# Performance work log

Measured on AMD Instinct MI355X. Metric: run time of the kernel, lower is better.

The kernel has to match this reference:

```python
import jax, jax.numpy as jnp
import numpy as np

E = 8        # num_experts (material buckets)
L1 = 3072    # input dim
L2 = 15
L3 = 32
RF = 32      # ROUTER_FEATURES_PER_PERSPECTIVE
B = 16384
AUX_ALPHA = 0.01
Z_ALPHA = 0.001
LOAD_FLOOR = 0.05
LOAD_CAP = 0.5
PROBE_ALPHA = 0.01
PROBE_TAU = 1.0
PROBE_THRESH = 0.05
TEACHER_ALPHA = 0.0   # initial value of _teacher_alpha buffer
SCORE_SCALE = 600.0
SQ_SCALE = 255.0 / 256.0


def setup_inputs() -> dict:
    key = jax.random.key(0)
    ks = jax.random.split(key, 12)
    x = jax.random.uniform(ks[0], (B, L1), dtype=jnp.float32)
    ls_indices = jax.random.randint(ks[1], (B,), 0, E)
    psqt = jax.random.normal(ks[2], (B,), dtype=jnp.float32)
    score_target = jax.random.normal(ks[3], (B,), dtype=jnp.float32)
    router_w = 0.1 * jax.random.normal(ks[4], (E, 2 * RF), dtype=jnp.float32)
    router_b = jnp.zeros((E,), dtype=jnp.float32)
    # effective (coalesced) expert params, per _expert_params view
    w1 = jax.random.normal(ks[5], (E, L2 + 1, L1), dtype=jnp.float32) / np.sqrt(L1)
    b1 = 0.01 * jax.random.normal(ks[6], (E, L2 + 1), dtype=jnp.float32)
    w2 = jax.random.normal(ks[7], (E, L3, 2 * L2), dtype=jnp.float32) / np.sqrt(2 * L2)
    b2 = 0.01 * jax.random.normal(ks[8], (E, L3), dtype=jnp.float32)
    w3 = jax.random.normal(ks[9], (E, 1, L3), dtype=jnp.float32) / np.sqrt(L3)
    b3 = jnp.zeros((E, 1), dtype=jnp.float32)  # output bias zeroed in __init__
    return {"x": x, "ls_indices": ls_indices, "psqt": psqt,
            "score_target": score_target, "router_w": router_w,
            "router_b": router_b, "w1": w1, "b1": b1, "w2": w2, "b2": b2,
            "w3": w3, "b3": b3}


def _forward(x, psqt, score_target, router_w, router_b, w1, b1, w2, b2, w3, b3, ls_indices):
    half = L1 // 2
    router_in = jnp.concatenate([x[:, :RF], x[:, half:half + RF]], axis=1)  # [B, 64]
    gate_logits = router_in @ router_w.T + router_b                          # [B, E]
    logp = jax.nn.log_softmax(gate_logits, axis=-1)
    gate_probs = jnp.exp(logp)
    expert_indices = jnp.argmax(gate_logits, axis=-1)                        # [B]

    teacher_ce = -jnp.mean(jnp.take_along_axis(logp, ls_indices[:, None], axis=1))
    frac = jnp.bincount(expert_indices, length=E).astype(gate_probs.dtype) / gate_probs.shape[0]
    avg_gate = gate_probs.mean(axis=0)
    load = avg_gate + jax.lax.stop_gradient(frac - avg_gate)
    floor_loss = jnp.mean(jnp.square(jnp.maximum(LOAD_FLOOR - load, 0.0)))
    cap_loss = jnp.mean(jnp.square(jnp.maximum(load - LOAD_CAP, 0.0)))
    aux_loss = floor_loss + cap_loss
    z_loss = jnp.mean(jnp.square(jax.nn.logsumexp(gate_logits, axis=-1)))

    # ---- all-experts stacked MLP (fusion target) ----
    l1c = jnp.einsum('bi,eoi->beo', x, w1) + b1          # [B, E, L2+1]
    a, a_skip = l1c[..., :L2], l1c[..., L2:]              # [B,E,L2], [B,E,1]
    h = jnp.clip(jnp.concatenate([a * a * SQ_SCALE, a], axis=-1), 0.0, 1.0)  # [B,E,2*L2]
    l2x = jnp.clip(jnp.einsum('bei,eoi->beo', h, w2) + b2, 0.0, 1.0)         # [B,E,L3]
    all_out = jnp.einsum('bei,eoi->beo', l2x, w3) + b3 + a_skip              # [B,E,1]

    # ---- probe loss ----
    probe_weight = PROBE_ALPHA * max(PROBE_THRESH - TEACHER_ALPHA, 0.0) / max(PROBE_THRESH, 1e-9)
    expert_out = (all_out[..., 0] + psqt[:, None]) * SCORE_SCALE             # [B, E]
    err = jnp.square(expert_out - score_target[:, None])
    err = err - err.min(axis=1, keepdims=True)
    pt = jax.nn.softmax(-jax.lax.stop_gradient(err) / PROBE_TAU, axis=-1)
    log_pt = jnp.log(jnp.maximum(pt, 1e-30))
    probe_loss = jnp.mean(jnp.sum(pt * (log_pt - logp), axis=-1))            # kl_div batchmean

    router_loss = (AUX_ALPHA * aux_loss + Z_ALPHA * z_loss
                   + TEACHER_ALPHA * teacher_ce + probe_weight * probe_loss)

    l3x = jnp.take_along_axis(all_out, expert_indices[:, None, None], axis=1)[:, 0, :]  # [B, 1]
    gp = jnp.take_along_axis(gate_probs, expert_indices[:, None], axis=1)               # [B, 1]
    l3x = l3x * (1.0 + gp - jax.lax.stop_gradient(gp))  # straight-through (training mode)
    return l3x, router_loss


def reference(x, ls_indices, psqt, score_target, router_w, router_b, w1, b1, w2, b2, w3, b3):
    return _forward(x, psqt, score_target, router_w, router_b, w1, b1, w2, b2, w3, b3, ls_indices)
```

## Files before the change

kernel.cpp:

```cpp
#include <hip/hip_runtime.h>
#include <math.h>

#define BATCH 16384
#define K_DIM 3072

typedef float  f32x4  __attribute__((ext_vector_type(4)));
typedef __bf16 bf16x8 __attribute__((ext_vector_type(8)));
typedef unsigned int u32x2 __attribute__((ext_vector_type(2)));

__device__ __forceinline__ unsigned short f2bf(float f) {
  union { float f; unsigned u; } v; v.f = f;
  unsigned u = v.u + 0x7fffu + ((v.u >> 16) & 1u);
  return (unsigned short)(u >> 16);
}

__device__ __forceinline__ bf16x8 cvt8(f32x4 lo, f32x4 hi) {
  bf16x8 r;
  r[0] = (__bf16)lo[0]; r[1] = (__bf16)lo[1]; r[2] = (__bf16)lo[2]; r[3] = (__bf16)lo[3];
  r[4] = (__bf16)hi[0]; r[5] = (__bf16)hi[1]; r[6] = (__bf16)hi[2]; r[7] = (__bf16)hi[3];
  return r;
}

__device__ __forceinline__ void gld16(const void* g, void* l) {
  __builtin_amdgcn_global_load_lds(
      (const __attribute__((address_space(1))) unsigned int*)g,
      (__attribute__((address_space(3))) unsigned int*)l, 16, 0, 0);
}

__global__ void cvt_w1_kernel(const float* __restrict__ w1, unsigned short* __restrict__ o,
                              float* __restrict__ accs) {
  if (blockIdx.x == 0 && threadIdx.x < 16) accs[threadIdx.x] = 0.f;
  int i = blockIdx.x * 256 + threadIdx.x;
  f32x4 v = ((const f32x4*)w1)[i];
  u32x2 p = { (unsigned)f2bf(v.x) | ((unsigned)f2bf(v.y) << 16),
              (unsigned)f2bf(v.z) | ((unsigned)f2bf(v.w) << 16) };
  ((u32x2*)o)[i] = p;
}

__global__ __launch_bounds__(256, 2) void moe_main_kernel(
    const float* __restrict__ x, const unsigned short* __restrict__ w1bf,
    const float* __restrict__ b1, const float* __restrict__ w2,
    const float* __restrict__ b2, const float* __restrict__ w3,
    const float* __restrict__ b3, const float* __restrict__ psqt,
    const float* __restrict__ st, const float* __restrict__ rw,
    const float* __restrict__ rb, float* __restrict__ out,
    float* __restrict__ accs) {
  __shared__ __align__(16) unsigned char stage_sm[73728];
  __shared__ int   hist[8];
  __shared__ float zred[4], wred[4];

  const int tid = threadIdx.x;
  const int bm  = blockIdx.x;
  float* Cl  = (float*)stage_sm;
  float* w2s = (float*)(stage_sm + 17024);

  if (tid < 8) hist[tid] = 0;
  __syncthreads();

  const int lane = tid & 63, wv = tid >> 6;
  const int l16 = lane & 15, lq = lane >> 4;
  const int rt = wv & 1;
  const int cb = (wv >> 1) << 2;

  const float* gA[2]; int lA[2];
#pragma unroll
  for (int r = 0; r < 2; ++r) {
    int idx = r * 256 + tid; int row = idx >> 4; int blk = idx & 15;
    gA[r] = x + (size_t)(bm * 32 + row) * K_DIM + ((blk ^ (row & 7)) << 2);
    lA[r] = idx << 4;
  }
  const unsigned short* gB[4]; int lB[4];
#pragma unroll
  for (int r = 0; r < 4; ++r) {
    int idx = r * 256 + tid; int row = idx >> 3; int blk = idx & 7;
    gB[r] = w1bf + (size_t)row * K_DIM + ((blk ^ (row & 7)) << 3);
    lB[r] = idx << 4;
  }

  const int arow = rt * 16 + l16;
  int aoff[2], boff[2][4];
#pragma unroll
  for (int ks = 0; ks < 2; ++ks) {
    aoff[ks] = arow * 256 + (((ks * 8 + lq * 2) ^ (arow & 7)) << 4);
#pragma unroll
    for (int cc = 0; cc < 4; ++cc) {
      int o = (cb + cc) * 16 + l16;
      boff[ks][cc] = o * 128 + (((lq + ks * 4) ^ (l16 & 7)) << 4);
    }
  }

#define STAGE(C, KT) do {                                                  \
    unsigned char* ab_ = stage_sm + (C) * 24576;                           \
    unsigned char* bb_ = ab_ + 8192;                                       \
    gld16(gA[0] + (KT) * 64, ab_ + lA[0]);                                 \
    gld16(gA[1] + (KT) * 64, ab_ + lA[1]);                                 \
    gld16(gB[0] + (KT) * 64, bb_ + lB[0]);                                 \
    gld16(gB[1] + (KT) * 64, bb_ + lB[1]);                                 \
    gld16(gB[2] + (KT) * 64, bb_ + lB[2]);                                 \
    gld16(gB[3] + (KT) * 64, bb_ + lB[3]);                                 \
  } while (0)

#define COMPUTE(C) do {                                                    \
    const unsigned char* ab_ = stage_sm + (C) * 24576;                     \
    const unsigned char* bb_ = ab_ + 8192;                                 \
    _Pragma("unroll")                                                      \
    for (int ks = 0; ks < 2; ++ks) {                                       \
      f32x4 a0 = *(const f32x4*)(ab_ + aoff[ks]);                          \
      f32x4 a1 = *(const f32x4*)(ab_ + (aoff[ks] ^ 16));                   \
      bf16x8 af = cvt8(a0, a1);                                            \
      _Pragma("unroll")                                                    \
      for (int cc = 0; cc < 4; ++cc) {                                     \
        bf16x8 bfv = *(const bf16x8*)(bb_ + boff[ks][cc]);                 \
        acc[cc] = __builtin_amdgcn_mfma_f32_16x16x32_bf16(af, bfv,         \
                                                          acc[cc], 0,0,0); \
      }                                                                    \
    }                                                                      \
  } while (0)

#define PH(C, T) do {                                                      \
    STAGE(((C) + 2) % 3, (T) + 2);                                         \
    asm volatile("s_waitcnt vmcnt(12)" ::: "memory");                      \
    __builtin_amdgcn_s_barrier();                                          \
    COMPUTE(C);                                                            \
    __builtin_amdgcn_s_barrier();                                          \
  } while (0)

  f32x4 acc[4];
#pragma unroll
  for (int cc = 0; cc < 4; ++cc) acc[cc] = (f32x4){0.f, 0.f, 0.f, 0.f};

  STAGE(0, 0);
  STAGE(1, 1);

  const int bl = tid >> 3, e = tid & 7;
  const int bg = bm * 32 + bl;
  const float* xrow  = x + (size_t)bg * K_DIM;
  const float* rwrow = rw + e * 64;
  double lr = (double)rb[e];
#pragma unroll
  for (int c4 = 0; c4 < 8; ++c4) {
    f32x4 xv = *(const f32x4*)(xrow + c4 * 4);
    f32x4 wvv = *(const f32x4*)(rwrow + c4 * 4);
#pragma unroll
    for (int j = 0; j < 4; ++j) lr = fma((double)xv[j], (double)wvv[j], lr);
  }
#pragma unroll
  for (int c4 = 0; c4 < 8; ++c4) {
    f32x4 xv = *(const f32x4*)(xrow + 1536 + c4 * 4);
    f32x4 wvv = *(const f32x4*)(rwrow + 32 + c4 * 4);
#pragma unroll
    for (int j = 0; j < 4; ++j) lr = fma((double)xv[j], (double)wvv[j], lr);
  }
  double mx = lr; int mi = e;
#pragma unroll
  for (int m = 1; m < 8; m <<= 1) {
    double ov = __shfl_xor(mx, m);
    int    oi = __shfl_xor(mi, m);
    if (ov > mx || (ov == mx && oi < mi)) { mx = ov; mi = oi; }
  }
  double ssum = exp(lr - mx);
#pragma unroll
  for (int m = 1; m < 8; m <<= 1) ssum += __shfl_xor(ssum, m);
  const double lse = mx + log(ssum);
  const float  logp_self = (float)(lr - lse);
  const int    rowEidx   = mi;

  if (e == 0) atomicAdd(&hist[rowEidx], 1);
  float zc = (e == 0) ? (float)(lse * lse) : 0.f;
#pragma unroll
  for (int m = 1; m < 64; m <<= 1) zc += __shfl_xor(zc, m);
  if (lane == 0) zred[wv] = zc;

#pragma unroll 1
  for (int kt = 0; kt < 45; kt += 3) {
    PH(0, kt);
    PH(1, kt + 1);
    PH(2, kt + 2);
  }
  PH(0, 45);
  asm volatile("s_waitcnt vmcnt(6)" ::: "memory");
  __builtin_amdgcn_s_barrier();
  COMPUTE(1);
  __builtin_amdgcn_s_barrier();
  asm volatile("s_waitcnt vmcnt(0)" ::: "memory");
  __builtin_amdgcn_s_barrier();
  COMPUTE(2);
  __builtin_amdgcn_s_barrier();

#pragma unroll
  for (int cc = 0; cc < 4; ++cc)
#pragma unroll
    for (int r = 0; r < 4; ++r)
      Cl[(rt * 16 + lq * 4 + r) * 132 + (cb + cc) * 16 + l16] = acc[cc][r];
  for (int i = tid; i < 7680; i += 256) {
    int ee = i / 960; int rr = i - ee * 960; int o = rr / 30; int ii = rr - o * 30;
    w2s[ee * 964 + ii * 32 + o] = w2[i];
  }
  __syncthreads();

  float a[16];
  {
    const float* crow = Cl + bl * 132 + e * 16;
    const float* b1p  = b1 + e * 16;
#pragma unroll
    for (int j = 0; j < 16; ++j) a[j] = crow[j] + b1p[j];
  }

  float h[30];
#pragma unroll
  for (int j = 0; j < 15; ++j) {
    float v = a[j];
    h[j]      = fminf(fmaxf(v * v * (255.0f / 256.0f), 0.f), 1.f);
    h[15 + j] = fminf(fmaxf(v, 0.f), 1.f);
  }

  float acc2[32];
  {
    const f32x4* b2v = (const f32x4*)(b2 + e * 32);
#pragma unroll
    for (int o4 = 0; o4 < 8; ++o4) {
      f32x4 t = b2v[o4];
      acc2[o4 * 4 + 0] = t.x; acc2[o4 * 4 + 1] = t.y;
      acc2[o4 * 4 + 2] = t.z; acc2[o4 * 4 + 3] = t.w;
    }
  }
  const f32x4* wrow = (const f32x4*)&w2s[e * 964];
#pragma unroll
  for (int i = 0; i < 30; ++i) {
    float hv = h[i];
#pragma unroll
    for (int o4 = 0; o4 < 8; ++o4) {
      f32x4 wq = wrow[i * 8 + o4];
      acc2[o4 * 4 + 0] += hv * wq.x;
      acc2[o4 * 4 + 1] += hv * wq.y;
      acc2[o4 * 4 + 2] += hv * wq.z;
      acc2[o4 * 4 + 3] += hv * wq.w;
    }
  }

  float outv = b3[e] + a[15];
  {
    const f32x4* w3v = (const f32x4*)(w3 + e * 32);
#pragma unroll
    for (int o4 = 0; o4 < 8; ++o4) {
      f32x4 t = w3v[o4];
      outv += fminf(fmaxf(acc2[o4 * 4 + 0], 0.f), 1.f) * t.x;
      outv += fminf(fmaxf(acc2[o4 * 4 + 1], 0.f), 1.f) * t.y;
      outv += fminf(fmaxf(acc2[o4 * 4 + 2], 0.f), 1.f) * t.z;
      outv += fminf(fmaxf(acc2[o4 * 4 + 3], 0.f), 1.f) * t.w;
    }
  }

  float eo  = (outv + psqt[bg]) * 600.0f;
  float dd  = eo - st[bg];
  float err = dd * dd;
  float mn = err;
  mn = fminf(mn, __shfl_xor(mn, 1));
  mn = fminf(mn, __shfl_xor(mn, 2));
  mn = fminf(mn, __shfl_xor(mn, 4));
  float wexp = expf(-(err - mn));
  float ss = wexp;
  ss += __shfl_xor(ss, 1); ss += __shfl_xor(ss, 2); ss += __shfl_xor(ss, 4);
  float pt  = wexp / ss;
  float lpt = logf(fmaxf(pt, 1e-30f));
  float term = pt * (lpt - logp_self);
  term += __shfl_xor(term, 1); term += __shfl_xor(term, 2); term += __shfl_xor(term, 4);
  float c1 = (e == 0) ? term : 0.f;
  c1 += __shfl_xor(c1, 8); c1 += __shfl_xor(c1, 16); c1 += __shfl_xor(c1, 32);
  if (lane == 0) wred[wv] = c1;

  if (e == rowEidx) out[bg] = outv;

  __syncthreads();
  if (tid == 0) {
    atomicAdd(&accs[8], zred[0] + zred[1] + zred[2] + zred[3]);
    atomicAdd(&accs[9], wred[0] + wred[1] + wred[2] + wred[3]);
  }
  if (tid < 8) atomicAdd(&accs[tid], (float)hist[tid]);
#undef STAGE
#undef COMPUTE
#undef PH
}

__global__ void finalize_kernel(const float* __restrict__ accs, float* __restrict__ out) {
  if (threadIdx.x == 0) {
    float fsum = 0.f;
    for (int e = 0; e < 8; ++e) {
      float frac = accs[e] * (1.0f / 16384.0f);
      float f = fmaxf(0.05f - frac, 0.f);
      float c = fmaxf(frac - 0.5f, 0.f);
      fsum += f * f + c * c;
    }
    float aux   = fsum * 0.125f;
    float z     = accs[8] * (1.0f / 16384.0f);
    float probe = accs[9] * (1.0f / 16384.0f);
    out[BATCH] = 0.01f * aux + 0.001f * z + 0.01f * probe;
  }
}

extern "C" void kernel_launch(void* const* d_in, const int* in_sizes, int n_in,
                              void* d_out, int out_size, void* d_ws, size_t ws_size,
                              hipStream_t stream) {
  const float* x    = (const float*)d_in[0];
  const float* psqt = (const float*)d_in[2];
  const float* st   = (const float*)d_in[3];
  const float* rw   = (const float*)d_in[4];
  const float* rb   = (const float*)d_in[5];
  const float* w1   = (const float*)d_in[6];
  const float* b1   = (const float*)d_in[7];
  const float* w2   = (const float*)d_in[8];
  const float* b2   = (const float*)d_in[9];
  const float* w3   = (const float*)d_in[10];
  const float* b3   = (const float*)d_in[11];
  float* out = (float*)d_out;

  unsigned short* w1bf = (unsigned short*)d_ws;
  float* accs = (float*)((char*)d_ws + 786432);

  cvt_w1_kernel<<<384, 256, 0, stream>>>(w1, w1bf, accs);
  moe_main_kernel<<<512, 256, 0, stream>>>(x, w1bf, b1, w2, b2, w3, b3,
                                           psqt, st, rw, rb, out, accs);
  finalize_kernel<<<1, 1, 0, stream>>>(accs, out);
}
```

Measured before the change: 332.3 us.

## Split block into producer and consumer warps for warp-specialized pipeline

Doubles the block to 512 threads: four producer waves issue the async global-to-LDS loads for the triple-buffered x/w1 tiles while four consumer waves run the MFMA compute and router. The point is to overlap memory issue with compute across separate waves instead of having every wave both load and compute. The cost is more threads per block, idle producer waves during the epilogue, and heavier register and occupancy pressure given the 72KB shared allocation. launch_bounds(512,4) cannot be met with that much LDS.

```diff
diff --git a/kernel.cpp b/kernel.cpp
--- a/kernel.cpp
+++ b/kernel.cpp
@@ -37,7 +37,7 @@
   ((u32x2*)o)[i] = p;
 }
 
-__global__ __launch_bounds__(256, 2) void moe_main_kernel(
+__global__ __launch_bounds__(512, 4) void moe_main_kernel(
     const float* __restrict__ x, const unsigned short* __restrict__ w1bf,
     const float* __restrict__ b1, const float* __restrict__ w2,
     const float* __restrict__ b2, const float* __restrict__ w3,
@@ -57,37 +57,15 @@
   if (tid < 8) hist[tid] = 0;
   __syncthreads();
 
-  const int lane = tid & 63, wv = tid >> 6;
-  const int l16 = lane & 15, lq = lane >> 4;
-  const int rt = wv & 1;
-  const int cb = (wv >> 1) << 2;
+  const int lane = tid & 63;
+  const bool isProd = (tid >= 256);
 
   const float* gA[2]; int lA[2];
-#pragma unroll
-  for (int r = 0; r < 2; ++r) {
-    int idx = r * 256 + tid; int row = idx >> 4; int blk = idx & 15;
-    gA[r] = x + (size_t)(bm * 32 + row) * K_DIM + ((blk ^ (row & 7)) << 2);
-    lA[r] = idx << 4;
-  }
   const unsigned short* gB[4]; int lB[4];
-#pragma unroll
-  for (int r = 0; r < 4; ++r) {
-    int idx = r * 256 + tid; int row = idx >> 3; int blk = idx & 7;
-    gB[r] = w1bf + (size_t)row * K_DIM + ((blk ^ (row & 7)) << 3);
-    lB[r] = idx << 4;
-  }
-
-  const int arow = rt * 16 + l16;
   int aoff[2], boff[2][4];
-#pragma unroll
-  for (int ks = 0; ks < 2; ++ks) {
-    aoff[ks] = arow * 256 + (((ks * 8 + lq * 2) ^ (arow & 7)) << 4);
-#pragma unroll
-    for (int cc = 0; cc < 4; ++cc) {
-      int o = (cb + cc) * 16 + l16;
-      boff[ks][cc] = o * 128 + (((lq + ks * 4) ^ (l16 & 7)) << 4);
-    }
-  }
+  f32x4 acc[4];
+  float logp_self = 0.f;
+  int   rowEidx   = 0;
 
 #define STAGE(C, KT) do {                                                  \
     unsigned char* ab_ = stage_sm + (C) * 24576;                           \
@@ -117,159 +95,196 @@
     }                                                                      \
   } while (0)
 
-#define PH(C, T) do {                                                      \
-    STAGE(((C) + 2) % 3, (T) + 2);                                         \
-    asm volatile("s_waitcnt vmcnt(12)" ::: "memory");                      \
-    __builtin_amdgcn_s_barrier();                                          \
-    COMPUTE(C);                                                            \
-    __builtin_amdgcn_s_barrier();                                          \
-  } while (0)
-
-  f32x4 acc[4];
-#pragma unroll
-  for (int cc = 0; cc < 4; ++cc) acc[cc] = (f32x4){0.f, 0.f, 0.f, 0.f};
-
-  STAGE(0, 0);
-  STAGE(1, 1);
-
-  const int bl = tid >> 3, e = tid & 7;
-  const int bg = bm * 32 + bl;
-  const float* xrow  = x + (size_t)bg * K_DIM;
-  const float* rwrow = rw + e * 64;
-  double lr = (double)rb[e];
-#pragma unroll
-  for (int c4 = 0; c4 < 8; ++c4) {
-    f32x4 xv = *(const f32x4*)(xrow + c4 * 4);
-    f32x4 wvv = *(const f32x4*)(rwrow + c4 * 4);
-#pragma unroll
-    for (int j = 0; j < 4; ++j) lr = fma((double)xv[j], (double)wvv[j], lr);
-  }
-#pragma unroll
-  for (int c4 = 0; c4 < 8; ++c4) {
-    f32x4 xv = *(const f32x4*)(xrow + 1536 + c4 * 4);
-    f32x4 wvv = *(const f32x4*)(rwrow + 32 + c4 * 4);
-#pragma unroll
-    for (int j = 0; j < 4; ++j) lr = fma((double)xv[j], (double)wvv[j], lr);
-  }
-  double mx = lr; int mi = e;
-#pragma unroll
-  for (int m = 1; m < 8; m <<= 1) {
-    double ov = __shfl_xor(mx, m);
-    int    oi = __shfl_xor(mi, m);
-    if (ov > mx || (ov == mx && oi < mi)) { mx = ov; mi = oi; }
-  }
-  double ssum = exp(lr - mx);
-#pragma unroll
-  for (int m = 1; m < 8; m <<= 1) ssum += __shfl_xor(ssum, m);
-  const double lse = mx + log(ssum);
-  const float  logp_self = (float)(lr - lse);
-  const int    rowEidx   = mi;
-
-  if (e == 0) atomicAdd(&hist[rowEidx], 1);
-  float zc = (e == 0) ? (float)(lse * lse) : 0.f;
-#pragma unroll
-  for (int m = 1; m < 64; m <<= 1) zc += __shfl_xor(zc, m);
-  if (lane == 0) zred[wv] = zc;
+  if (isProd) {
+    const int ptid = tid & 255;
+#pragma unroll
+    for (int r = 0; r < 2; ++r) {
+      int idx = r * 256 + ptid; int row = idx >> 4; int blk = idx & 15;
+      gA[r] = x + (size_t)(bm * 32 + row) * K_DIM + ((blk ^ (row & 7)) << 2);
+      lA[r] = idx << 4;
+    }
+#pragma unroll
+    for (int r = 0; r < 4; ++r) {
+      int idx = r * 256 + ptid; int row = idx >> 3; int blk = idx & 7;
+      gB[r] = w1bf + (size_t)row * K_DIM + ((blk ^ (row & 7)) << 3);
+      lB[r] = idx << 4;
+    }
+    STAGE(0, 0);
+    STAGE(1, 1);
+    asm volatile("s_waitcnt vmcnt(6)" ::: "memory");
+  } else {
+    const int cwv = tid >> 6;
+    const int l16 = lane & 15, lq = lane >> 4;
+    const int rt = cwv & 1;
+    const int cb = (cwv >> 1) << 2;
+    const int arow = rt * 16 + l16;
+#pragma unroll
+    for (int ks = 0; ks < 2; ++ks) {
+      aoff[ks] = arow * 256 + (((ks * 8 + lq * 2) ^ (arow & 7)) << 4);
+#pragma unroll
+      for (int cc = 0; cc < 4; ++cc) {
+        int o = (cb + cc) * 16 + l16;
+        boff[ks][cc] = o * 128 + (((lq + ks * 4) ^ (l16 & 7)) << 4);
+      }
+    }
+#pragma unroll
+    for (int cc = 0; cc < 4; ++cc) acc[cc] = (f32x4){0.f, 0.f, 0.f, 0.f};
+
+    const int bl = tid >> 3, e = tid & 7;
+    const int bg = bm * 32 + bl;
+    const float* xrow  = x + (size_t)bg * K_DIM;
+    const float* rwrow = rw + e * 64;
+    double lr = (double)rb[e];
+#pragma unroll
+    for (int c4 = 0; c4 < 8; ++c4) {
+      f32x4 xv  = *(const f32x4*)(xrow + c4 * 4);
+      f32x4 wvv = *(const f32x4*)(rwrow + c4 * 4);
+#pragma unroll
+      for (int j = 0; j < 4; ++j) lr = fma((double)xv[j], (double)wvv[j], lr);
+    }
+#pragma unroll
+    for (int c4 = 0; c4 < 8; ++c4) {
+      f32x4 xv  = *(const f32x4*)(xrow + 1536 + c4 * 4);
+      f32x4 wvv = *(const f32x4*)(rwrow + 32 + c4 * 4);
+#pragma unroll
+      for (int j = 0; j < 4; ++j) lr = fma((double)xv[j], (double)wvv[j], lr);
+    }
+    double mx = lr; int mi = e;
+#pragma unroll
+    for (int m = 1; m < 8; m <<= 1) {
+      double ov = __shfl_xor(mx, m);
+      int    oi = __shfl_xor(mi, m);
+      if (ov > mx || (ov == mx && oi < mi)) { mx = ov; mi = oi; }
+    }
+    double ssum = exp(lr - mx);
+#pragma unroll
+    for (int m = 1; m < 8; m <<= 1) ssum += __shfl_xor(ssum, m);
+    const double lse = mx + log(ssum);
+    logp_self = (float)(lr - lse);
+    rowEidx   = mi;
+
+    if (e == 0) atomicAdd(&hist[rowEidx], 1);
+    float zc = (e == 0) ? (float)(lse * lse) : 0.f;
+#pragma unroll
+    for (int m = 1; m < 64; m <<= 1) zc += __shfl_xor(zc, m);
+    if (lane == 0) zred[cwv] = zc;
+  }
 
 #pragma unroll 1
-  for (int kt = 0; kt < 45; kt += 3) {
-    PH(0, kt);
-    PH(1, kt + 1);
-    PH(2, kt + 2);
-  }
-  PH(0, 45);
-  asm volatile("s_waitcnt vmcnt(6)" ::: "memory");
+  for (int base = 0; base < 45; base += 3) {
+    __builtin_amdgcn_s_barrier();
+    if (isProd) { STAGE(2, base + 2); asm volatile("s_waitcnt vmcnt(6)" ::: "memory"); }
+    else        COMPUTE(0);
+    __builtin_amdgcn_s_barrier();
+    if (isProd) { STAGE(0, base + 3); asm volatile("s_waitcnt vmcnt(6)" ::: "memory"); }
+    else        COMPUTE(1);
+    __builtin_amdgcn_s_barrier();
+    if (isProd) { STAGE(1, base + 4); asm volatile("s_waitcnt vmcnt(6)" ::: "memory"); }
+    else        COMPUTE(2);
+  }
   __builtin_amdgcn_s_barrier();
-  COMPUTE(1);
+  if (isProd) { STAGE(2, 47); asm volatile("s_waitcnt vmcnt(6)" ::: "memory"); }
+  else        COMPUTE(0);
   __builtin_amdgcn_s_barrier();
-  asm volatile("s_waitcnt vmcnt(0)" ::: "memory");
+  if (isProd) { asm volatile("s_waitcnt vmcnt(0)" ::: "memory"); }
+  else        COMPUTE(1);
   __builtin_amdgcn_s_barrier();
-  COMPUTE(2);
-  __builtin_amdgcn_s_barrier();
-
-#pragma unroll
-  for (int cc = 0; cc < 4; ++cc)
-#pragma unroll
-    for (int r = 0; r < 4; ++r)
-      Cl[(rt * 16 + lq * 4 + r) * 132 + (cb + cc) * 16 + l16] = acc[cc][r];
-  for (int i = tid; i < 7680; i += 256) {
+  if (!isProd) COMPUTE(2);
+
+  __syncthreads();
+  if (!isProd) {
+    const int cwv = tid >> 6;
+    const int l16 = lane & 15, lq = lane >> 4;
+    const int rt = cwv & 1, cb = (cwv >> 1) << 2;
+#pragma unroll
+    for (int cc = 0; cc < 4; ++cc)
+#pragma unroll
+      for (int r = 0; r < 4; ++r)
+        Cl[(rt * 16 + lq * 4 + r) * 132 + (cb + cc) * 16 + l16] = acc[cc][r];
+  }
+  for (int i = tid; i < 7680; i += 512) {
     int ee = i / 960; int rr = i - ee * 960; int o = rr / 30; int ii = rr - o * 30;
     w2s[ee * 964 + ii * 32 + o] = w2[i];
   }
   __syncthreads();
 
-  float a[16];
-  {
-    const float* crow = Cl + bl * 132 + e * 16;
-    const float* b1p  = b1 + e * 16;
-#pragma unroll
-    for (int j = 0; j < 16; ++j) a[j] = crow[j] + b1p[j];
-  }
-
-  float h[30];
-#pragma unroll
-  for (int j = 0; j < 15; ++j) {
-    float v = a[j];
-    h[j]      = fminf(fmaxf(v * v * (255.0f / 256.0f), 0.f), 1.f);
-    h[15 + j] = fminf(fmaxf(v, 0.f), 1.f);
-  }
-
-  float acc2[32];
-  {
-    const f32x4* b2v = (const f32x4*)(b2 + e * 32);
-#pragma unroll
-    for (int o4 = 0; o4 < 8; ++o4) {
-      f32x4 t = b2v[o4];
-      acc2[o4 * 4 + 0] = t.x; acc2[o4 * 4 + 1] = t.y;
-      acc2[o4 * 4 + 2] = t.z; acc2[o4 * 4 + 3] = t.w;
-    }
-  }
-  const f32x4* wrow = (const f32x4*)&w2s[e * 964];
-#pragma unroll
-  for (int i = 0; i < 30; ++i) {
-    float hv = h[i];
-#pragma unroll
-    for (int o4 = 0; o4 < 8; ++o4) {
-      f32x4 wq = wrow[i * 8 + o4];
-      acc2[o4 * 4 + 0] += hv * wq.x;
-      acc2[o4 * 4 + 1] += hv * wq.y;
-      acc2[o4 * 4 + 2] += hv * wq.z;
-      acc2[o4 * 4 + 3] += hv * wq.w;
-    }
-  }
-
-  float outv = b3[e] + a[15];
-  {
-    const f32x4* w3v = (const f32x4*)(w3 + e * 32);
-#pragma unroll
-    for (int o4 = 0; o4 < 8; ++o4) {
-      f32x4 t = w3v[o4];
-      outv += fminf(fmaxf(acc2[o4 * 4 + 0], 0.f), 1.f) * t.x;
-      outv += fminf(fmaxf(acc2[o4 * 4 + 1], 0.f), 1.f) * t.y;
-      outv += fminf(fmaxf(acc2[o4 * 4 + 2], 0.f), 1.f) * t.z;
-      outv += fminf(fmaxf(acc2[o4 * 4 + 3], 0.f), 1.f) * t.w;
-    }
-  }
-
-  float eo  = (outv + psqt[bg]) * 600.0f;
-  float dd  = eo - st[bg];
-  float err = dd * dd;
-  float mn = err;
-  mn = fminf(mn, __shfl_xor(mn, 1));
-  mn = fminf(mn, __shfl_xor(mn, 2));
-  mn = fminf(mn, __shfl_xor(mn, 4));
-  float wexp = expf(-(err - mn));
-  float ss = wexp;
-  ss += __shfl_xor(ss, 1); ss += __shfl_xor(ss, 2); ss += __shfl_xor(ss, 4);
-  float pt  = wexp / ss;
-  float lpt = logf(fmaxf(pt, 1e-30f));
-  float term = pt * (lpt - logp_self);
-  term += __shfl_xor(term, 1); term += __shfl_xor(term, 2); term += __shfl_xor(term, 4);
-  float c1 = (e == 0) ? term : 0.f;
-  c1 += __shfl_xor(c1, 8); c1 += __shfl_xor(c1, 16); c1 += __shfl_xor(c1, 32);
-  if (lane == 0) wred[wv] = c1;
-
-  if (e == rowEidx) out[bg] = outv;
+  if (tid < 256) {
+    const int bl = tid >> 3, e = tid & 7;
+    const int bg = bm * 32 + bl;
+
+    float a[16];
+    {
+      const float* crow = Cl + bl * 132 + e * 16;
+      const float* b1p  = b1 + e * 16;
+#pragma unroll
+      for (int j = 0; j < 16; ++j) a[j] = crow[j] + b1p[j];
+    }
+
+    float h[30];
+#pragma unroll
+    for (int j = 0; j < 15; ++j) {
+      float v = a[j];
+      h[j]      = fminf(fmaxf(v * v * (255.0f / 256.0f), 0.f), 1.f);
+      h[15 + j] = fminf(fmaxf(v, 0.f), 1.f);
+    }
+
+    float acc2[32];
+    {
+      const f32x4* b2v = (const f32x4*)(b2 + e * 32);
+#pragma unroll
+      for (int o4 = 0; o4 < 8; ++o4) {
+        f32x4 t = b2v[o4];
+        acc2[o4 * 4 + 0] = t.x; acc2[o4 * 4 + 1] = t.y;
+        acc2[o4 * 4 + 2] = t.z; acc2[o4 * 4 + 3] = t.w;
+      }
+    }
+    const f32x4* wrow = (const f32x4*)&w2s[e * 964];
+#pragma unroll
+    for (int i = 0; i < 30; ++i) {
+      float hv = h[i];
+#pragma unroll
+      for (int o4 = 0; o4 < 8; ++o4) {
+        f32x4 wq = wrow[i * 8 + o4];
+        acc2[o4 * 4 + 0] += hv * wq.x;
+        acc2[o4 * 4 + 1] += hv * wq.y;
+        acc2[o4 * 4 + 2] += hv * wq.z;
+        acc2[o4 * 4 + 3] += hv * wq.w;
+      }
+    }
+
+    float outv = b3[e] + a[15];
+    {
+      const f32x4* w3v = (const f32x4*)(w3 + e * 32);
+#pragma unroll
+      for (int o4 = 0; o4 < 8; ++o4) {
+        f32x4 t = w3v[o4];
+        outv += fminf(fmaxf(acc2[o4 * 4 + 0], 0.f), 1.f) * t.x;
+        outv += fminf(fmaxf(acc2[o4 * 4 + 1], 0.f), 1.f) * t.y;
+        outv += fminf(fmaxf(acc2[o4 * 4 + 2], 0.f), 1.f) * t.z;
+        outv += fminf(fmaxf(acc2[o4 * 4 + 3], 0.f), 1.f) * t.w;
+      }
+    }
+
+    float eo  = (outv + psqt[bg]) * 600.0f;
+    float dd  = eo - st[bg];
+    float err = dd * dd;
+    float mn = err;
+    mn = fminf(mn, __shfl_xor(mn, 1));
+    mn = fminf(mn, __shfl_xor(mn, 2));
+    mn = fminf(mn, __shfl_xor(mn, 4));
+    float wexp = expf(-(err - mn));
+    float ss = wexp;
+    ss += __shfl_xor(ss, 1); ss += __shfl_xor(ss, 2); ss += __shfl_xor(ss, 4);
+    float pt  = wexp / ss;
+    float lpt = logf(fmaxf(pt, 1e-30f));
+    float term = pt * (lpt - logp_self);
+    term += __shfl_xor(term, 1); term += __shfl_xor(term, 2); term += __shfl_xor(term, 4);
+    float c1 = (e == 0) ? term : 0.f;
+    c1 += __shfl_xor(c1, 8); c1 += __shfl_xor(c1, 16); c1 += __shfl_xor(c1, 32);
+    if (lane == 0) wred[tid >> 6] = c1;
+
+    if (e == rowEidx) out[bg] = outv;
+  }
 
   __syncthreads();
   if (tid == 0) {
@@ -279,7 +294,6 @@
   if (tid < 8) atomicAdd(&accs[tid], (float)hist[tid]);
 #undef STAGE
 #undef COMPUTE
-#undef PH
 }
 
 __global__ void finalize_kernel(const float* __restrict__ accs, float* __restrict__ out) {
@@ -318,7 +332,7 @@
   float* accs = (float*)((char*)d_ws + 786432);
 
   cvt_w1_kernel<<<384, 256, 0, stream>>>(w1, w1bf, accs);
-  moe_main_kernel<<<512, 256, 0, stream>>>(x, w1bf, b1, w2, b2, w3, b3,
+  moe_main_kernel<<<512, 512, 0, stream>>>(x, w1bf, b1, w2, b2, w3, b3,
                                            psqt, st, rw, rb, out, accs);
   finalize_kernel<<<1, 1, 0, stream>>>(accs, out);
 }
```

Measured after the change: 327.4 us. Within noise of the previous version (-1.5%).

## Halve row tile to 16, double-buffer pipeline, and raise occupancy to four blocks

Applied to the files above, without the earlier changes.

Shrinks each block's batch tile from 32 to 16 rows and launches twice as many blocks. It replaces the triple-buffered LDS pipeline with a double buffer, cutting shared memory so four blocks can fit per CU. The shared-memory histogram and reductions are replaced by direct global atomics. The aim is more parallelism and better latency hiding on a memory-bound GEMM over x. In exchange, each w1 tile is reloaded by twice as many blocks, there are more global atomics, half the threads sit idle in the epilogue, and prefetch depth is reduced.

```diff
diff --git a/kernel.cpp b/kernel.cpp
--- a/kernel.cpp
+++ b/kernel.cpp
@@ -37,7 +37,7 @@
   ((u32x2*)o)[i] = p;
 }
 
-__global__ __launch_bounds__(256, 2) void moe_main_kernel(
+__global__ __launch_bounds__(256, 4) void moe_main_kernel(
     const float* __restrict__ x, const unsigned short* __restrict__ w1bf,
     const float* __restrict__ b1, const float* __restrict__ w2,
     const float* __restrict__ b2, const float* __restrict__ w3,
@@ -45,29 +45,22 @@
     const float* __restrict__ st, const float* __restrict__ rw,
     const float* __restrict__ rb, float* __restrict__ out,
     float* __restrict__ accs) {
-  __shared__ __align__(16) unsigned char stage_sm[73728];
-  __shared__ int   hist[8];
-  __shared__ float zred[4], wred[4];
+  __shared__ __align__(16) unsigned char stage_sm[40960];
 
   const int tid = threadIdx.x;
   const int bm  = blockIdx.x;
   float* Cl  = (float*)stage_sm;
-  float* w2s = (float*)(stage_sm + 17024);
-
-  if (tid < 8) hist[tid] = 0;
-  __syncthreads();
+  float* w2s = (float*)(stage_sm + 8448);
 
   const int lane = tid & 63, wv = tid >> 6;
   const int l16 = lane & 15, lq = lane >> 4;
-  const int rt = wv & 1;
-  const int cb = (wv >> 1) << 2;
-
-  const float* gA[2]; int lA[2];
-#pragma unroll
-  for (int r = 0; r < 2; ++r) {
-    int idx = r * 256 + tid; int row = idx >> 4; int blk = idx & 15;
-    gA[r] = x + (size_t)(bm * 32 + row) * K_DIM + ((blk ^ (row & 7)) << 2);
-    lA[r] = idx << 4;
+  const int cb = wv << 1;
+
+  const float* gA; int lA;
+  {
+    int row = tid >> 4, blk = tid & 15;
+    gA = x + (size_t)(bm * 16 + row) * K_DIM + ((blk ^ (row & 7)) << 2);
+    lA = tid << 4;
   }
   const unsigned short* gB[4]; int lB[4];
 #pragma unroll
@@ -77,23 +70,21 @@
     lB[r] = idx << 4;
   }
 
-  const int arow = rt * 16 + l16;
-  int aoff[2], boff[2][4];
+  int aoff[2], boff[2][2];
 #pragma unroll
   for (int ks = 0; ks < 2; ++ks) {
-    aoff[ks] = arow * 256 + (((ks * 8 + lq * 2) ^ (arow & 7)) << 4);
-#pragma unroll
-    for (int cc = 0; cc < 4; ++cc) {
+    aoff[ks] = l16 * 256 + (((ks * 8 + lq * 2) ^ (l16 & 7)) << 4);
+#pragma unroll
+    for (int cc = 0; cc < 2; ++cc) {
       int o = (cb + cc) * 16 + l16;
       boff[ks][cc] = o * 128 + (((lq + ks * 4) ^ (l16 & 7)) << 4);
     }
   }
 
 #define STAGE(C, KT) do {                                                  \
-    unsigned char* ab_ = stage_sm + (C) * 24576;                           \
-    unsigned char* bb_ = ab_ + 8192;                                       \
-    gld16(gA[0] + (KT) * 64, ab_ + lA[0]);                                 \
-    gld16(gA[1] + (KT) * 64, ab_ + lA[1]);                                 \
+    unsigned char* ab_ = stage_sm + (C) * 20480;                           \
+    unsigned char* bb_ = ab_ + 4096;                                       \
+    gld16(gA + (KT) * 64, ab_ + lA);                                       \
     gld16(gB[0] + (KT) * 64, bb_ + lB[0]);                                 \
     gld16(gB[1] + (KT) * 64, bb_ + lB[1]);                                 \
     gld16(gB[2] + (KT) * 64, bb_ + lB[2]);                                 \
@@ -101,15 +92,15 @@
   } while (0)
 
 #define COMPUTE(C) do {                                                    \
-    const unsigned char* ab_ = stage_sm + (C) * 24576;                     \
-    const unsigned char* bb_ = ab_ + 8192;                                 \
+    const unsigned char* ab_ = stage_sm + (C) * 20480;                     \
+    const unsigned char* bb_ = ab_ + 4096;                                 \
     _Pragma("unroll")                                                      \
     for (int ks = 0; ks < 2; ++ks) {                                       \
       f32x4 a0 = *(const f32x4*)(ab_ + aoff[ks]);                          \
       f32x4 a1 = *(const f32x4*)(ab_ + (aoff[ks] ^ 16));                   \
       bf16x8 af = cvt8(a0, a1);                                            \
       _Pragma("unroll")                                                    \
-      for (int cc = 0; cc < 4; ++cc) {                                     \
+      for (int cc = 0; cc < 2; ++cc) {                                     \
         bf16x8 bfv = *(const bf16x8*)(bb_ + boff[ks][cc]);                 \
         acc[cc] = __builtin_amdgcn_mfma_f32_16x16x32_bf16(af, bfv,         \
                                                           acc[cc], 0,0,0); \
@@ -117,169 +108,158 @@
     }                                                                      \
   } while (0)
 
-#define PH(C, T) do {                                                      \
-    STAGE(((C) + 2) % 3, (T) + 2);                                         \
-    asm volatile("s_waitcnt vmcnt(12)" ::: "memory");                      \
-    __builtin_amdgcn_s_barrier();                                          \
-    COMPUTE(C);                                                            \
-    __builtin_amdgcn_s_barrier();                                          \
-  } while (0)
-
-  f32x4 acc[4];
-#pragma unroll
-  for (int cc = 0; cc < 4; ++cc) acc[cc] = (f32x4){0.f, 0.f, 0.f, 0.f};
+  f32x4 acc[2];
+  acc[0] = (f32x4){0.f, 0.f, 0.f, 0.f};
+  acc[1] = (f32x4){0.f, 0.f, 0.f, 0.f};
 
   STAGE(0, 0);
-  STAGE(1, 1);
-
-  const int bl = tid >> 3, e = tid & 7;
-  const int bg = bm * 32 + bl;
-  const float* xrow  = x + (size_t)bg * K_DIM;
-  const float* rwrow = rw + e * 64;
-  double lr = (double)rb[e];
-#pragma unroll
-  for (int c4 = 0; c4 < 8; ++c4) {
-    f32x4 xv = *(const f32x4*)(xrow + c4 * 4);
-    f32x4 wvv = *(const f32x4*)(rwrow + c4 * 4);
-#pragma unroll
-    for (int j = 0; j < 4; ++j) lr = fma((double)xv[j], (double)wvv[j], lr);
-  }
-#pragma unroll
-  for (int c4 = 0; c4 < 8; ++c4) {
-    f32x4 xv = *(const f32x4*)(xrow + 1536 + c4 * 4);
-    f32x4 wvv = *(const f32x4*)(rwrow + 32 + c4 * 4);
-#pragma unroll
-    for (int j = 0; j < 4; ++j) lr = fma((double)xv[j], (double)wvv[j], lr);
-  }
-  double mx = lr; int mi = e;
-#pragma unroll
-  for (int m = 1; m < 8; m <<= 1) {
-    double ov = __shfl_xor(mx, m);
-    int    oi = __shfl_xor(mi, m);
-    if (ov > mx || (ov == mx && oi < mi)) { mx = ov; mi = oi; }
-  }
-  double ssum = exp(lr - mx);
-#pragma unroll
-  for (int m = 1; m < 8; m <<= 1) ssum += __shfl_xor(ssum, m);
-  const double lse = mx + log(ssum);
-  const float  logp_self = (float)(lr - lse);
-  const int    rowEidx   = mi;
-
-  if (e == 0) atomicAdd(&hist[rowEidx], 1);
-  float zc = (e == 0) ? (float)(lse * lse) : 0.f;
-#pragma unroll
-  for (int m = 1; m < 64; m <<= 1) zc += __shfl_xor(zc, m);
-  if (lane == 0) zred[wv] = zc;
+
+  float logp_self = 0.f;
+  int   rowEidx   = 0;
+  if (tid < 128) {
+    const int bl = tid >> 3, e = tid & 7;
+    const int bg = bm * 16 + bl;
+    const float* xrow  = x + (size_t)bg * K_DIM;
+    const float* rwrow = rw + e * 64;
+    double lr = (double)rb[e];
+#pragma unroll
+    for (int c4 = 0; c4 < 8; ++c4) {
+      f32x4 xv  = *(const f32x4*)(xrow + c4 * 4);
+      f32x4 wvv = *(const f32x4*)(rwrow + c4 * 4);
+#pragma unroll
+      for (int j = 0; j < 4; ++j) lr = fma((double)xv[j], (double)wvv[j], lr);
+    }
+#pragma unroll
+    for (int c4 = 0; c4 < 8; ++c4) {
+      f32x4 xv  = *(const f32x4*)(xrow + 1536 + c4 * 4);
+      f32x4 wvv = *(const f32x4*)(rwrow + 32 + c4 * 4);
+#pragma unroll
+      for (int j = 0; j < 4; ++j) lr = fma((double)xv[j], (double)wvv[j], lr);
+    }
+    double mx = lr; int mi = e;
+#pragma unroll
+    for (int m = 1; m < 8; m <<= 1) {
+      double ov = __shfl_xor(mx, m);
+      int    oi = __shfl_xor(mi, m);
+      if (ov > mx || (ov == mx && oi < mi)) { mx = ov; mi = oi; }
+    }
+    double ssum = exp(lr - mx);
+#pragma unroll
+    for (int m = 1; m < 8; m <<= 1) ssum += __shfl_xor(ssum, m);
+    const double lse = mx + log(ssum);
+    logp_self = (float)(lr - lse);
+    rowEidx   = mi;
+
+    if (e == 0) atomicAdd(&accs[rowEidx], 1.0f);
+    float zc = (e == 0) ? (float)(lse * lse) : 0.f;
+#pragma unroll
+    for (int m = 1; m < 64; m <<= 1) zc += __shfl_xor(zc, m);
+    if (lane == 0) atomicAdd(&accs[8], zc);
+  }
 
 #pragma unroll 1
-  for (int kt = 0; kt < 45; kt += 3) {
-    PH(0, kt);
-    PH(1, kt + 1);
-    PH(2, kt + 2);
-  }
-  PH(0, 45);
-  asm volatile("s_waitcnt vmcnt(6)" ::: "memory");
+  for (int t = 0; t < 47; ++t) {
+    STAGE((t + 1) & 1, t + 1);
+    asm volatile("s_waitcnt vmcnt(5)" ::: "memory");
+    __builtin_amdgcn_s_barrier();
+    COMPUTE(t & 1);
+    __builtin_amdgcn_s_barrier();
+  }
+  asm volatile("s_waitcnt vmcnt(0)" ::: "memory");
   __builtin_amdgcn_s_barrier();
   COMPUTE(1);
-  __builtin_amdgcn_s_barrier();
-  asm volatile("s_waitcnt vmcnt(0)" ::: "memory");
-  __builtin_amdgcn_s_barrier();
-  COMPUTE(2);
-  __builtin_amdgcn_s_barrier();
-
-#pragma unroll
-  for (int cc = 0; cc < 4; ++cc)
+
+  __syncthreads();
+#pragma unroll
+  for (int cc = 0; cc < 2; ++cc)
 #pragma unroll
     for (int r = 0; r < 4; ++r)
-      Cl[(rt * 16 + lq * 4 + r) * 132 + (cb + cc) * 16 + l16] = acc[cc][r];
+      Cl[(lq * 4 + r) * 132 + (cb + cc) * 16 + l16] = acc[cc][r];
   for (int i = tid; i < 7680; i += 256) {
     int ee = i / 960; int rr = i - ee * 960; int o = rr / 30; int ii = rr - o * 30;
     w2s[ee * 964 + ii * 32 + o] = w2[i];
   }
   __syncthreads();
 
-  float a[16];
-  {
-    const float* crow = Cl + bl * 132 + e * 16;
-    const float* b1p  = b1 + e * 16;
-#pragma unroll
-    for (int j = 0; j < 16; ++j) a[j] = crow[j] + b1p[j];
-  }
-
-  float h[30];
-#pragma unroll
-  for (int j = 0; j < 15; ++j) {
-    float v = a[j];
-    h[j]      = fminf(fmaxf(v * v * (255.0f / 256.0f), 0.f), 1.f);
-    h[15 + j] = fminf(fmaxf(v, 0.f), 1.f);
-  }
-
-  float acc2[32];
-  {
-    const f32x4* b2v = (const f32x4*)(b2 + e * 32);
-#pragma unroll
-    for (int o4 = 0; o4 < 8; ++o4) {
-      f32x4 t = b2v[o4];
-      acc2[o4 * 4 + 0] = t.x; acc2[o4 * 4 + 1] = t.y;
-      acc2[o4 * 4 + 2] = t.z; acc2[o4 * 4 + 3] = t.w;
-    }
-  }
-  const f32x4* wrow = (const f32x4*)&w2s[e * 964];
-#pragma unroll
-  for (int i = 0; i < 30; ++i) {
-    float hv = h[i];
-#pragma unroll
-    for (int o4 = 0; o4 < 8; ++o4) {
-      f32x4 wq = wrow[i * 8 + o4];
-      acc2[o4 * 4 + 0] += hv * wq.x;
-      acc2[o4 * 4 + 1] += hv * wq.y;
-      acc2[o4 * 4 + 2] += hv * wq.z;
-      acc2[o4 * 4 + 3] += hv * wq.w;
-    }
-  }
-
-  float outv = b3[e] + a[15];
-  {
-    const f32x4* w3v = (const f32x4*)(w3 + e * 32);
-#pragma unroll
-    for (int o4 = 0; o4 < 8; ++o4) {
-      f32x4 t = w3v[o4];
-      outv += fminf(fmaxf(acc2[o4 * 4 + 0], 0.f), 1.f) * t.x;
-      outv += fminf(fmaxf(acc2[o4 * 4 + 1], 0.f), 1.f) * t.y;
-      outv += fminf(fmaxf(acc2[o4 * 4 + 2], 0.f), 1.f) * t.z;
-      outv += fminf(fmaxf(acc2[o4 * 4 + 3], 0.f), 1.f) * t.w;
-    }
-  }
-
-  float eo  = (outv + psqt[bg]) * 600.0f;
-  float dd  = eo - st[bg];
-  float err = dd * dd;
-  float mn = err;
-  mn = fminf(mn, __shfl_xor(mn, 1));
-  mn = fminf(mn, __shfl_xor(mn, 2));
-  mn = fminf(mn, __shfl_xor(mn, 4));
-  float wexp = expf(-(err - mn));
-  float ss = wexp;
-  ss += __shfl_xor(ss, 1); ss += __shfl_xor(ss, 2); ss += __shfl_xor(ss, 4);
-  float pt  = wexp / ss;
-  float lpt = logf(fmaxf(pt, 1e-30f));
-  float term = pt * (lpt - logp_self);
-  term += __shfl_xor(term, 1); term += __shfl_xor(term, 2); term += __shfl_xor(term, 4);
-  float c1 = (e == 0) ? term : 0.f;
-  c1 += __shfl_xor(c1, 8); c1 += __shfl_xor(c1, 16); c1 += __shfl_xor(c1, 32);
-  if (lane == 0) wred[wv] = c1;
-
-  if (e == rowEidx) out[bg] = outv;
-
-  __syncthreads();
-  if (tid == 0) {
-    atomicAdd(&accs[8], zred[0] + zred[1] + zred[2] + zred[3]);
-    atomicAdd(&accs[9], wred[0] + wred[1] + wred[2] + wred[3]);
-  }
-  if (tid < 8) atomicAdd(&accs[tid], (float)hist[tid]);
+  if (tid < 128) {
+    const int bl = tid >> 3, e = tid & 7;
+    const int bg = bm * 16 + bl;
+
+    float a[16];
+    {
+      const float* crow = Cl + bl * 132 + e * 16;
+      const float* b1p  = b1 + e * 16;
+#pragma unroll
+      for (int j = 0; j < 16; ++j) a[j] = crow[j] + b1p[j];
+    }
+
+    float h[30];
+#pragma unroll
+    for (int j = 0; j < 15; ++j) {
+      float v = a[j];
+      h[j]      = fminf(fmaxf(v * v * (255.0f / 256.0f), 0.f), 1.f);
+      h[15 + j] = fminf(fmaxf(v, 0.f), 1.f);
+    }
+
+    float acc2[32];
+    {
+      const f32x4* b2v = (const f32x4*)(b2 + e * 32);
+#pragma unroll
+      for (int o4 = 0; o4 < 8; ++o4) {
+        f32x4 tv = b2v[o4];
+        acc2[o4 * 4 + 0] = tv.x; acc2[o4 * 4 + 1] = tv.y;
+        acc2[o4 * 4 + 2] = tv.z; acc2[o4 * 4 + 3] = tv.w;
+      }
+    }
+    const f32x4* wrow = (const f32x4*)&w2s[e * 964];
+#pragma unroll
+    for (int i = 0; i < 30; ++i) {
+      float hv = h[i];
+#pragma unroll
+      for (int o4 = 0; o4 < 8; ++o4) {
+        f32x4 wq = wrow[i * 8 + o4];
+        acc2[o4 * 4 + 0] += hv * wq.x;
+        acc2[o4 * 4 + 1] += hv * wq.y;
+        acc2[o4 * 4 + 2] += hv * wq.z;
+        acc2[o4 * 4 + 3] += hv * wq.w;
+      }
+    }
+
+    float outv = b3[e] + a[15];
+    {
+      const f32x4* w3v = (const f32x4*)(w3 + e * 32);
+#pragma unroll
+      for (int o4 = 0; o4 < 8; ++o4) {
+        f32x4 tv = w3v[o4];
+        outv += fminf(fmaxf(acc2[o4 * 4 + 0], 0.f), 1.f) * tv.x;
+        outv += fminf(fmaxf(acc2[o4 * 4 + 1], 0.f), 1.f) * tv.y;
+        outv += fminf(fmaxf(acc2[o4 * 4 + 2], 0.f), 1.f) * tv.z;
+        outv += fminf(fmaxf(acc2[o4 * 4 + 3], 0.f), 1.f) * tv.w;
+      }
+    }
+
+    float eo  = (outv + psqt[bg]) * 600.0f;
+    float dd  = eo - st[bg];
+    float err = dd * dd;
+    float mn = err;
+    mn = fminf(mn, __shfl_xor(mn, 1));
+    mn = fminf(mn, __shfl_xor(mn, 2));
+    mn = fminf(mn, __shfl_xor(mn, 4));
+    float wexp = expf(-(err - mn));
+    float ss = wexp;
+    ss += __shfl_xor(ss, 1); ss += __shfl_xor(ss, 2); ss += __shfl_xor(ss, 4);
+    float pt  = wexp / ss;
+    float lpt = logf(fmaxf(pt, 1e-30f));
+    float term = pt * (lpt - logp_self);
+    term += __shfl_xor(term, 1); term += __shfl_xor(term, 2); term += __shfl_xor(term, 4);
+    float c1 = (e == 0) ? term : 0.f;
+    c1 += __shfl_xor(c1, 8); c1 += __shfl_xor(c1, 16); c1 += __shfl_xor(c1, 32);
+    if (lane == 0) atomicAdd(&accs[9], c1);
+
+    if (e == rowEidx) out[bg] = outv;
+  }
 #undef STAGE
 #undef COMPUTE
-#undef PH
 }
 
 __global__ void finalize_kernel(const float* __restrict__ accs, float* __restrict__ out) {
@@ -318,7 +298,7 @@
   float* accs = (float*)((char*)d_ws + 786432);
 
   cvt_w1_kernel<<<384, 256, 0, stream>>>(w1, w1bf, accs);
-  moe_main_kernel<<<512, 256, 0, stream>>>(x, w1bf, b1, w2, b2, w3, b3,
-                                           psqt, st, rw, rb, out, accs);
+  moe_main_kernel<<<1024, 256, 0, stream>>>(x, w1bf, b1, w2, b2, w3, b3,
+                                            psqt, st, rw, rb, out, accs);
   finalize_kernel<<<1, 1, 0, stream>>>(accs, out);
 }
```

Result: slower. 492.2 us (+48.1%).
